# Kernel optimization log

Hardware: AMD Instinct MI355X
Metric: run time of the kernel (lower is better)

Reference implementation:

```python
import jax, jax.numpy as jnp
import numpy as np


def setup_inputs() -> dict:
    key = jax.random.key(0)
    k1, k2 = jax.random.split(key)
    L, B, H = 1024, 64, 1024
    encoder_outputs = jax.random.normal(k1, (L, B, H), dtype=jnp.float32)
    decoder_gru_out = jax.random.normal(k2, (1, B, H), dtype=jnp.float32)
    return {"encoder_outputs": encoder_outputs, "decoder_gru_out": decoder_gru_out}


def reference(encoder_outputs, decoder_gru_out):
    # scores[l,b] = sum_h enc[l,b,h] * dec[0,b,h]
    scores = jnp.einsum('lbh,bh->lb', encoder_outputs, decoder_gru_out[0])
    # softmax over the sequence (L) axis
    attn = jax.nn.softmax(scores, axis=0)  # [L, B]
    # context[b,h] = sum_l attn[l,b] * enc[l,b,h]
    context = jnp.einsum('lb,lbh->bh', attn, encoder_outputs)
    return context
```

## Files before the change

### kernel.cpp

```cpp
#include <hip/hip_runtime.h>
#include <math.h>

#define L_SEQ 1024
#define BATCH 64
#define HDIM  1024
#define WPB   4

#define LOG2E 1.44269504088896340736f

__global__ __launch_bounds__(256) void attn_partial_kernel(
    const float* __restrict__ enc, const float* __restrict__ dec,
    float* __restrict__ wsC, float* __restrict__ wsML,
    int split, int chunk)
{
    const int tid  = threadIdx.x;
    const int lane = tid & 63;
    const int wave = tid >> 6;
    const int w    = blockIdx.x * WPB + wave;
    const int b    = w / split;
    const int k    = w - b * split;
    const int l0   = k * chunk;

    const float4* decv = (const float4*)(dec + (size_t)b * HDIM);
    float4 d[4];
    #pragma unroll
    for (int q = 0; q < 4; ++q) d[q] = decv[lane + 64 * q];

    float m = -INFINITY;
    float lsum = 0.0f;
    float4 a[4];
    #pragma unroll
    for (int q = 0; q < 4; ++q) a[q] = make_float4(0.f, 0.f, 0.f, 0.f);

    const size_t row_stride = (size_t)BATCH * HDIM;

    for (int g = 0; g < chunk; g += 4) {
        const float* base = enc + ((size_t)(l0 + g) * BATCH + b) * HDIM;

        float4 e[4][4];
        #pragma unroll
        for (int r = 0; r < 4; ++r) {
            const float4* row = (const float4*)(base + r * row_stride);
            #pragma unroll
            for (int q = 0; q < 4; ++q) e[r][q] = row[lane + 64 * q];
        }

        float p[4];
        #pragma unroll
        for (int r = 0; r < 4; ++r) {
            float s = 0.0f;
            #pragma unroll
            for (int q = 0; q < 4; ++q) {
                s = fmaf(e[r][q].x, d[q].x, s);
                s = fmaf(e[r][q].y, d[q].y, s);
                s = fmaf(e[r][q].z, d[q].z, s);
                s = fmaf(e[r][q].w, d[q].w, s);
            }
            p[r] = s;
        }

        #pragma unroll
        for (int off = 32; off > 0; off >>= 1) {
            p[0] += __shfl_xor(p[0], off, 64);
            p[1] += __shfl_xor(p[1], off, 64);
            p[2] += __shfl_xor(p[2], off, 64);
            p[3] += __shfl_xor(p[3], off, 64);
        }

        const float s0 = p[0] * LOG2E, s1 = p[1] * LOG2E;
        const float s2 = p[2] * LOG2E, s3 = p[3] * LOG2E;
        const float mn = fmaxf(m, fmaxf(fmaxf(s0, s1), fmaxf(s2, s3)));
        const float scale = exp2f(m - mn);
        const float w0 = exp2f(s0 - mn);
        const float w1 = exp2f(s1 - mn);
        const float w2 = exp2f(s2 - mn);
        const float w3 = exp2f(s3 - mn);
        m = mn;
        lsum = fmaf(lsum, scale, (w0 + w1) + (w2 + w3));

        #pragma unroll
        for (int q = 0; q < 4; ++q) {
            a[q].x = fmaf(w3, e[3][q].x, fmaf(w2, e[2][q].x, fmaf(w1, e[1][q].x, fmaf(w0, e[0][q].x, a[q].x * scale))));
            a[q].y = fmaf(w3, e[3][q].y, fmaf(w2, e[2][q].y, fmaf(w1, e[1][q].y, fmaf(w0, e[0][q].y, a[q].y * scale))));
            a[q].z = fmaf(w3, e[3][q].z, fmaf(w2, e[2][q].z, fmaf(w1, e[1][q].z, fmaf(w0, e[0][q].z, a[q].z * scale))));
            a[q].w = fmaf(w3, e[3][q].w, fmaf(w2, e[2][q].w, fmaf(w1, e[1][q].w, fmaf(w0, e[0][q].w, a[q].w * scale))));
        }
    }

    const size_t r = (size_t)b * split + k;
    float4* C = (float4*)(wsC + r * (size_t)HDIM);
    #pragma unroll
    for (int q = 0; q < 4; ++q) C[lane + 64 * q] = a[q];
    if (lane == 0) {
        wsML[2 * r]     = m;
        wsML[2 * r + 1] = lsum;
    }
}

__global__ __launch_bounds__(256) void attn_reduce_kernel(
    const float* __restrict__ wsC, const float* __restrict__ wsML,
    float* __restrict__ out, int split)
{
    const int b = blockIdx.x >> 2;
    const int q = blockIdx.x & 3;
    const int h = q * 256 + threadIdx.x;

    float M = -INFINITY;
    for (int k = 0; k < split; ++k)
        M = fmaxf(M, wsML[2 * ((size_t)b * split + k)]);

    float Ltot = 0.0f;
    float acc = 0.0f;
    for (int k = 0; k < split; ++k) {
        const size_t r = (size_t)b * split + k;
        const float wgt = exp2f(wsML[2 * r] - M);
        Ltot = fmaf(wsML[2 * r + 1], wgt, Ltot);
        acc = fmaf(wsC[r * (size_t)HDIM + h], wgt, acc);
    }
    out[(size_t)b * HDIM + h] = acc / Ltot;
}

extern "C" void kernel_launch(void* const* d_in, const int* in_sizes, int n_in,
                              void* d_out, int out_size, void* d_ws, size_t ws_size,
                              hipStream_t stream) {
    const float* enc = (const float*)d_in[0];
    const float* dec = (const float*)d_in[1];
    float* out = (float*)d_out;

    int split = 64;
    while (split > 1) {
        const size_t need = (size_t)BATCH * split * HDIM * sizeof(float)
                          + (size_t)BATCH * split * 2 * sizeof(float);
        if (need <= ws_size) break;
        split >>= 1;
    }
    const int chunk = L_SEQ / split;

    float* wsC  = (float*)d_ws;
    float* wsML = wsC + (size_t)BATCH * split * HDIM;

    const int nblocks = (BATCH * split) / WPB;
    attn_partial_kernel<<<nblocks, 256, 0, stream>>>(enc, dec, wsC, wsML, split, chunk);
    attn_reduce_kernel<<<BATCH * 4, 256, 0, stream>>>(wsC, wsML, out, split);
}
```

Measured before the change: 380.9 us.

## Double-buffer encoder row loads, template split sizes, and skip redundant rescaling

The split and chunk sizes become template parameters, and the split rises to 128 when the workspace allows, with a fallback to 16. The partial kernel now works on 2 rows per step and prefetches the next pair into a second register buffer while the current pair is computed, to hide load latency. Accumulators are rescaled only when the running max grows, and the launch bounds request 4 blocks per CU. The larger split doubles the workspace traffic and the work done by the reduce kernel, and the fallback path ignores workspace sizes between 16 and 128.

```diff
diff --git a/kernel.cpp b/kernel.cpp
--- a/kernel.cpp
+++ b/kernel.cpp
@@ -8,18 +8,19 @@
 
 #define LOG2E 1.44269504088896340736f
 
-__global__ __launch_bounds__(256) void attn_partial_kernel(
+template <int SPLIT, int CHUNK>
+__global__ __launch_bounds__(256, 4) void attn_partial_kernel(
     const float* __restrict__ enc, const float* __restrict__ dec,
-    float* __restrict__ wsC, float* __restrict__ wsML,
-    int split, int chunk)
+    float* __restrict__ wsC, float* __restrict__ wsML)
 {
+    constexpr int NG = CHUNK / 2;
     const int tid  = threadIdx.x;
     const int lane = tid & 63;
     const int wave = tid >> 6;
     const int w    = blockIdx.x * WPB + wave;
-    const int b    = w / split;
-    const int k    = w - b * split;
-    const int l0   = k * chunk;
+    const int b    = w / SPLIT;
+    const int k    = w - b * SPLIT;
+    const int l0   = k * CHUNK;
 
     const float4* decv = (const float4*)(dec + (size_t)b * HDIM);
     float4 d[4];
@@ -33,61 +34,78 @@
     for (int q = 0; q < 4; ++q) a[q] = make_float4(0.f, 0.f, 0.f, 0.f);
 
     const size_t row_stride = (size_t)BATCH * HDIM;
+    const float* base0 = enc + ((size_t)l0 * BATCH + b) * HDIM;
 
-    for (int g = 0; g < chunk; g += 4) {
-        const float* base = enc + ((size_t)(l0 + g) * BATCH + b) * HDIM;
+    float4 R[2][2][4];
 
-        float4 e[4][4];
+    #pragma unroll
+    for (int r = 0; r < 2; ++r) {
+        const float4* row = (const float4*)(base0 + r * row_stride);
         #pragma unroll
-        for (int r = 0; r < 4; ++r) {
-            const float4* row = (const float4*)(base + r * row_stride);
+        for (int q = 0; q < 4; ++q) R[0][r][q] = row[lane + 64 * q];
+    }
+
+    #pragma unroll
+    for (int g = 0; g < NG; ++g) {
+        const int buf = g & 1;
+
+        if (g + 1 < NG) {
+            const float* nbase = base0 + (size_t)(2 * (g + 1)) * row_stride;
             #pragma unroll
-            for (int q = 0; q < 4; ++q) e[r][q] = row[lane + 64 * q];
+            for (int r = 0; r < 2; ++r) {
+                const float4* row = (const float4*)(nbase + r * row_stride);
+                #pragma unroll
+                for (int q = 0; q < 4; ++q) R[buf ^ 1][r][q] = row[lane + 64 * q];
+            }
         }
 
-        float p[4];
+        float p0 = 0.0f, p1 = 0.0f;
         #pragma unroll
-        for (int r = 0; r < 4; ++r) {
-            float s = 0.0f;
-            #pragma unroll
-            for (int q = 0; q < 4; ++q) {
-                s = fmaf(e[r][q].x, d[q].x, s);
-                s = fmaf(e[r][q].y, d[q].y, s);
-                s = fmaf(e[r][q].z, d[q].z, s);
-                s = fmaf(e[r][q].w, d[q].w, s);
-            }
-            p[r] = s;
+        for (int q = 0; q < 4; ++q) {
+            p0 = fmaf(R[buf][0][q].x, d[q].x, p0);
+            p0 = fmaf(R[buf][0][q].y, d[q].y, p0);
+            p0 = fmaf(R[buf][0][q].z, d[q].z, p0);
+            p0 = fmaf(R[buf][0][q].w, d[q].w, p0);
+            p1 = fmaf(R[buf][1][q].x, d[q].x, p1);
+            p1 = fmaf(R[buf][1][q].y, d[q].y, p1);
+            p1 = fmaf(R[buf][1][q].z, d[q].z, p1);
+            p1 = fmaf(R[buf][1][q].w, d[q].w, p1);
         }
 
         #pragma unroll
         for (int off = 32; off > 0; off >>= 1) {
-            p[0] += __shfl_xor(p[0], off, 64);
-            p[1] += __shfl_xor(p[1], off, 64);
-            p[2] += __shfl_xor(p[2], off, 64);
-            p[3] += __shfl_xor(p[3], off, 64);
+            p0 += __shfl_xor(p0, off, 64);
+            p1 += __shfl_xor(p1, off, 64);
         }
 
-        const float s0 = p[0] * LOG2E, s1 = p[1] * LOG2E;
-        const float s2 = p[2] * LOG2E, s3 = p[3] * LOG2E;
-        const float mn = fmaxf(m, fmaxf(fmaxf(s0, s1), fmaxf(s2, s3)));
-        const float scale = exp2f(m - mn);
-        const float w0 = exp2f(s0 - mn);
-        const float w1 = exp2f(s1 - mn);
-        const float w2 = exp2f(s2 - mn);
-        const float w3 = exp2f(s3 - mn);
-        m = mn;
-        lsum = fmaf(lsum, scale, (w0 + w1) + (w2 + w3));
+        const float s0 = p0 * LOG2E;
+        const float s1 = p1 * LOG2E;
+        const float gm = fmaxf(s0, s1);
 
+        if (gm > m) {
+            const float scale = exp2f(m - gm);
+            lsum *= scale;
+            #pragma unroll
+            for (int q = 0; q < 4; ++q) {
+                a[q].x *= scale;  a[q].y *= scale;
+                a[q].z *= scale;  a[q].w *= scale;
+            }
+            m = gm;
+        }
+
+        const float w0 = exp2f(s0 - m);
+        const float w1 = exp2f(s1 - m);
+        lsum += w0 + w1;
         #pragma unroll
         for (int q = 0; q < 4; ++q) {
-            a[q].x = fmaf(w3, e[3][q].x, fmaf(w2, e[2][q].x, fmaf(w1, e[1][q].x, fmaf(w0, e[0][q].x, a[q].x * scale))));
-            a[q].y = fmaf(w3, e[3][q].y, fmaf(w2, e[2][q].y, fmaf(w1, e[1][q].y, fmaf(w0, e[0][q].y, a[q].y * scale))));
-            a[q].z = fmaf(w3, e[3][q].z, fmaf(w2, e[2][q].z, fmaf(w1, e[1][q].z, fmaf(w0, e[0][q].z, a[q].z * scale))));
-            a[q].w = fmaf(w3, e[3][q].w, fmaf(w2, e[2][q].w, fmaf(w1, e[1][q].w, fmaf(w0, e[0][q].w, a[q].w * scale))));
+            a[q].x = fmaf(w1, R[buf][1][q].x, fmaf(w0, R[buf][0][q].x, a[q].x));
+            a[q].y = fmaf(w1, R[buf][1][q].y, fmaf(w0, R[buf][0][q].y, a[q].y));
+            a[q].z = fmaf(w1, R[buf][1][q].z, fmaf(w0, R[buf][0][q].z, a[q].z));
+            a[q].w = fmaf(w1, R[buf][1][q].w, fmaf(w0, R[buf][0][q].w, a[q].w));
         }
     }
 
-    const size_t r = (size_t)b * split + k;
+    const size_t r = (size_t)b * SPLIT + k;
     float4* C = (float4*)(wsC + r * (size_t)HDIM);
     #pragma unroll
     for (int q = 0; q < 4; ++q) C[lane + 64 * q] = a[q];
@@ -127,19 +145,21 @@
     const float* dec = (const float*)d_in[1];
     float* out = (float*)d_out;
 
-    int split = 64;
-    while (split > 1) {
-        const size_t need = (size_t)BATCH * split * HDIM * sizeof(float)
-                          + (size_t)BATCH * split * 2 * sizeof(float);
-        if (need <= ws_size) break;
-        split >>= 1;
+    const size_t need128 = (size_t)BATCH * 128 * HDIM * sizeof(float)
+                         + (size_t)BATCH * 128 * 2 * sizeof(float);
+    float* wsC = (float*)d_ws;
+
+    if (ws_size >= need128) {
+        constexpr int SPLIT = 128, CHUNK = L_SEQ / 128;
+        float* wsML = wsC + (size_t)BATCH * SPLIT * HDIM;
+        attn_partial_kernel<SPLIT, CHUNK>
+            <<<(BATCH * SPLIT) / WPB, 256, 0, stream>>>(enc, dec, wsC, wsML);
+        attn_reduce_kernel<<<BATCH * 4, 256, 0, stream>>>(wsC, wsML, out, SPLIT);
+    } else {
+        constexpr int SPLIT = 16, CHUNK = L_SEQ / 16;
+        float* wsML = wsC + (size_t)BATCH * SPLIT * HDIM;
+        attn_partial_kernel<SPLIT, CHUNK>
+            <<<(BATCH * SPLIT) / WPB, 256, 0, stream>>>(enc, dec, wsC, wsML);
+        attn_reduce_kernel<<<BATCH * 4, 256, 0, stream>>>(wsC, wsML, out, SPLIT);
     }
-    const int chunk = L_SEQ / split;
-
-    float* wsC  = (float*)d_ws;
-    float* wsML = wsC + (size_t)BATCH * split * HDIM;
-
-    const int nblocks = (BATCH * split) / WPB;
-    attn_partial_kernel<<<nblocks, 256, 0, stream>>>(enc, dec, wsC, wsML, split, chunk);
-    attn_reduce_kernel<<<BATCH * 4, 256, 0, stream>>>(wsC, wsML, out, split);
 }
```

After: 401.3 us. 5.3% more time.
